# Performance work log

Measured on AMD Instinct MI355X. Metric: run time of the kernel, lower is better.

Reference implementation:

```python
import jax, jax.numpy as jnp
import numpy as np

NUM_LEVELS = 3      # init: nums_levels
SAMPLE_POINTS = 9   # init: sample_points (S+1 = 10 samples per level)


def _ste_ceil(x):
    # straight-through ceil: forward ceil(x), gradient identity
    return jnp.ceil(x) - jax.lax.stop_gradient(x) + x


def _ste_floor(x):
    return jnp.floor(x) - jax.lax.stop_gradient(x) + x


def _local_cost_volume(cv, cur_disp, radius, sample_nums):
    # cv: [B,D,H,W], cur_disp: [B,1,H,W]
    B, D, H, W = cv.shape
    lower = cur_disp - radius                                   # [B,1,H,W]
    interval = (2.0 * radius) / sample_nums                     # scalar (upper-lower)/S
    steps = jnp.arange(sample_nums + 1, dtype=cv.dtype).reshape(1, -1, 1, 1)
    cand = lower + steps * interval                             # [B,S+1,H,W]
    ceil_c = jnp.clip(_ste_ceil(cand), 0, D - 1)
    floor_c = jnp.clip(_ste_floor(cand), 0, D - 1)
    floor_rate = ceil_c - cand
    ceil_rate = 1.0 - floor_rate
    idx_c = jax.lax.stop_gradient(ceil_c).astype(jnp.int32)
    idx_f = jax.lax.stop_gradient(floor_c).astype(jnp.int32)
    vol_c = jnp.take_along_axis(cv, idx_c, axis=1)              # gather along D
    vol_f = jnp.take_along_axis(cv, idx_f, axis=1)
    return vol_c * ceil_rate + vol_f * floor_rate               # [B,S+1,H,W]


def setup_inputs() -> dict:
    key = jax.random.key(0)
    k1, k2 = jax.random.split(key)
    B, D, H, W = 16, 64, 128, 240
    cost_volume = jax.random.normal(k1, (B, D, H, W), dtype=jnp.float32)
    # current disparity estimate in [0, D-1)
    cur_disp = jax.random.uniform(k2, (B, 1, H, W), dtype=jnp.float32) * (D - 1)
    return {"cost_volume": cost_volume, "radius": 4, "cur_disp": cur_disp}


def reference(cost_volume, radius, cur_disp):
    # Build pyramid by pairwise averaging along the disparity dim
    # (equivalent to the permute + avg_pool1d(2,2) + permute in the original).
    pyramid = [cost_volume]
    cv = cost_volume
    for _ in range(NUM_LEVELS - 1):
        B, D, H, W = cv.shape
        cv = cv.reshape(B, D // 2, 2, H, W).mean(axis=2)
        pyramid.append(cv)
    outs = []
    for i in range(NUM_LEVELS):
        ref_disp = cur_disp / (2.0 ** i)
        outs.append(_local_cost_volume(pyramid[i], ref_disp, float(radius), SAMPLE_POINTS))
    return jnp.concatenate(outs, axis=1)  # [B, NUM_LEVELS*(S+1), H, W]
```

## Files before the change

### kernel.cpp

```cpp
#include <hip/hip_runtime.h>
#include <hip/hip_fp16.h>

#define BB 16
#define DD 64
#define HH 128
#define WW 240
#define HW (HH * WW)
#define NS 10
#define NL 3
#define BLK 256
#define NWORD (DD / 2)

__device__ inline unsigned pack2h(float lo, float hi) {
    __half2 h = __floats2half2_rn(lo, hi);
    return *reinterpret_cast<unsigned*>(&h);
}
__device__ inline float2 unpack2h(unsigned u) {
    __half2 h = *reinterpret_cast<__half2*>(&u);
    return __half22float2(h);
}
__device__ inline float exth(unsigned u, int sel) {
    unsigned short us = (unsigned short)(u >> (sel << 4));
    __half_raw hr; hr.x = us;
    return __half2float(*reinterpret_cast<__half*>(&hr));
}

__global__ __launch_bounds__(BLK, 4) void pcv_kernel(
    const float* __restrict__ cv,
    const int* __restrict__ radius_p,
    const float* __restrict__ disp_in,
    float* __restrict__ out)
{
    __shared__ unsigned ldsw[NWORD * BLK];
    const int tid = threadIdx.x;
    const int p = blockIdx.x * BLK + tid;
    const int b = p / HW;
    const int pix = p - b * HW;

    const float disp = disp_in[p];

    const float r = (float)(*radius_p);
    const float interval = (float)((2.0 * (double)r) / 9.0);

    {
        const int pixbase = blockIdx.x * BLK - b * HW;
        const float* src = cv + (size_t)b * DD * HW + pixbase;
        const int q = tid & 63;
        const int jbase = tid >> 6;
        #pragma unroll
        for (int it = 0; it < 8; ++it) {
            const int j = it * 4 + jbase;
            float4 v0 = *reinterpret_cast<const float4*>(src + (size_t)(2 * j)     * HW + q * 4);
            float4 v1 = *reinterpret_cast<const float4*>(src + (size_t)(2 * j + 1) * HW + q * 4);
            uint4 wv;
            wv.x = pack2h(v0.x, v1.x);
            wv.y = pack2h(v0.y, v1.y);
            wv.z = pack2h(v0.z, v1.z);
            wv.w = pack2h(v0.w, v1.w);
            *reinterpret_cast<uint4*>(&ldsw[j * BLK + q * 4]) = wv;
        }
    }
    __syncthreads();

    float* outp = out + (size_t)b * (NL * NS) * HW + pix;

    float rd = disp;
    int Dl = DD;
    #pragma unroll
    for (int lvl = 0; lvl < NL; ++lvl) {
        const float lower = rd - r;
        const float dmax = (float)(Dl - 1);
        #pragma unroll
        for (int s = 0; s < NS; ++s) {
            float cand = lower + (float)s * interval;
            float cc = fminf(fmaxf(ceilf(cand),  0.0f), dmax);
            float fc = fminf(fmaxf(floorf(cand), 0.0f), dmax);
            float fr = cc - cand;
            float cr = 1.0f - fr;
            int ic = (int)cc;
            int fi = (int)fc;
            float vc, vf;
            if (lvl == 0) {
                unsigned uf = ldsw[(fi >> 1) * BLK + tid];
                unsigned uc = ldsw[(ic >> 1) * BLK + tid];
                vf = exth(uf, fi & 1);
                vc = exth(uc, ic & 1);
            } else if (lvl == 1) {
                float2 a = unpack2h(ldsw[fi * BLK + tid]);
                float2 c = unpack2h(ldsw[ic * BLK + tid]);
                vf = 0.5f * (a.x + a.y);
                vc = 0.5f * (c.x + c.y);
            } else {
                float2 a0 = unpack2h(ldsw[(2 * fi)     * BLK + tid]);
                float2 a1 = unpack2h(ldsw[(2 * fi + 1) * BLK + tid]);
                float2 c0 = unpack2h(ldsw[(2 * ic)     * BLK + tid]);
                float2 c1 = unpack2h(ldsw[(2 * ic + 1) * BLK + tid]);
                vf = 0.5f * (0.5f * (a0.x + a0.y) + 0.5f * (a1.x + a1.y));
                vc = 0.5f * (0.5f * (c0.x + c0.y) + 0.5f * (c1.x + c1.y));
            }
            outp[(size_t)(lvl * NS + s) * HW] = vc * cr + vf * fr;
        }
        rd *= 0.5f;
        Dl >>= 1;
    }
}

extern "C" void kernel_launch(void* const* d_in, const int* in_sizes, int n_in,
                              void* d_out, int out_size, void* d_ws, size_t ws_size,
                              hipStream_t stream) {
    const float* cv     = (const float*)d_in[0];
    const int*   radius = (const int*)  d_in[1];
    const float* disp   = (const float*)d_in[2];
    float*       out    = (float*)d_out;

    const int npix = BB * HH * WW;
    pcv_kernel<<<dim3(npix / BLK), dim3(BLK), 0, stream>>>(cv, radius, disp, out);
}
```

Baseline: 34.65 us.

## Make kernel persistent with register prefetch and double-buffered LDS tiles

Launches a fixed grid of 512 blocks that loop over pixel tiles. While the current tile is computed from one LDS buffer, the next tile's cost-volume slice and disparity are loaded into registers, and they are packed into the other LDS buffer on the following iteration. This aims to overlap global loads with the gather/interpolate and store phase. In exchange it doubles LDS per block, holds 64 extra registers for prefetch, and has uneven tile counts per block.

Result: slower. 37.32 us (+7.7%).

```diff
diff --git a/kernel.cpp b/kernel.cpp
--- a/kernel.cpp
+++ b/kernel.cpp
@@ -10,6 +10,8 @@
 #define NL 3
 #define BLK 256
 #define NWORD (DD / 2)
+#define GRID 512
+#define NTILE (BB * HW / BLK)
 
 __device__ inline unsigned pack2h(float lo, float hi) {
     __half2 h = __floats2half2_rn(lo, hi);
@@ -25,83 +27,119 @@
     return __half2float(*reinterpret_cast<__half*>(&hr));
 }
 
-__global__ __launch_bounds__(BLK, 4) void pcv_kernel(
+__global__ __launch_bounds__(BLK) void pcv_kernel(
     const float* __restrict__ cv,
     const int* __restrict__ radius_p,
     const float* __restrict__ disp_in,
     float* __restrict__ out)
 {
-    __shared__ unsigned ldsw[NWORD * BLK];
+    __shared__ unsigned ldsw[2][NWORD * BLK];
     const int tid = threadIdx.x;
-    const int p = blockIdx.x * BLK + tid;
-    const int b = p / HW;
-    const int pix = p - b * HW;
-
-    const float disp = disp_in[p];
+    const int bid = blockIdx.x;
+    const int q  = tid & 63;
+    const int jb = tid >> 6;
 
     const float r = (float)(*radius_p);
     const float interval = (float)((2.0 * (double)r) / 9.0);
 
+    const int ntiles = (NTILE - bid + GRID - 1) / GRID;
+
+    float4 rv[16];
+    float  dsp;
+
     {
-        const int pixbase = blockIdx.x * BLK - b * HW;
+        const int t = bid;
+        const int pb = t * BLK;
+        const int b = pb / HW;
+        const int pixbase = pb - b * HW;
         const float* src = cv + (size_t)b * DD * HW + pixbase;
-        const int q = tid & 63;
-        const int jbase = tid >> 6;
         #pragma unroll
         for (int it = 0; it < 8; ++it) {
-            const int j = it * 4 + jbase;
-            float4 v0 = *reinterpret_cast<const float4*>(src + (size_t)(2 * j)     * HW + q * 4);
-            float4 v1 = *reinterpret_cast<const float4*>(src + (size_t)(2 * j + 1) * HW + q * 4);
+            const int j = it * 4 + jb;
+            rv[2 * it]     = *reinterpret_cast<const float4*>(src + (size_t)(2 * j)     * HW + q * 4);
+            rv[2 * it + 1] = *reinterpret_cast<const float4*>(src + (size_t)(2 * j + 1) * HW + q * 4);
+        }
+        dsp = disp_in[pb + tid];
+    }
+
+    int cur = 0;
+    for (int k = 0; k < ntiles; ++k) {
+        const int t = bid + k * GRID;
+        const int pb = t * BLK;
+        const int b = pb / HW;
+        const int pix = pb - b * HW + tid;
+
+        unsigned* buf = &ldsw[cur][0];
+        #pragma unroll
+        for (int it = 0; it < 8; ++it) {
+            const int j = it * 4 + jb;
             uint4 wv;
-            wv.x = pack2h(v0.x, v1.x);
-            wv.y = pack2h(v0.y, v1.y);
-            wv.z = pack2h(v0.z, v1.z);
-            wv.w = pack2h(v0.w, v1.w);
-            *reinterpret_cast<uint4*>(&ldsw[j * BLK + q * 4]) = wv;
+            wv.x = pack2h(rv[2 * it].x, rv[2 * it + 1].x);
+            wv.y = pack2h(rv[2 * it].y, rv[2 * it + 1].y);
+            wv.z = pack2h(rv[2 * it].z, rv[2 * it + 1].z);
+            wv.w = pack2h(rv[2 * it].w, rv[2 * it + 1].w);
+            *reinterpret_cast<uint4*>(&buf[j * BLK + q * 4]) = wv;
         }
-    }
-    __syncthreads();
+        const float disp = dsp;
 
-    float* outp = out + (size_t)b * (NL * NS) * HW + pix;
+        if (k + 1 < ntiles) {
+            const int tn = bid + (k + 1) * GRID;
+            const int pbn = tn * BLK;
+            const int bn = pbn / HW;
+            const int pixbase_n = pbn - bn * HW;
+            const float* srcn = cv + (size_t)bn * DD * HW + pixbase_n;
+            #pragma unroll
+            for (int it = 0; it < 8; ++it) {
+                const int j = it * 4 + jb;
+                rv[2 * it]     = *reinterpret_cast<const float4*>(srcn + (size_t)(2 * j)     * HW + q * 4);
+                rv[2 * it + 1] = *reinterpret_cast<const float4*>(srcn + (size_t)(2 * j + 1) * HW + q * 4);
+            }
+            dsp = disp_in[pbn + tid];
+        }
 
-    float rd = disp;
-    int Dl = DD;
-    #pragma unroll
-    for (int lvl = 0; lvl < NL; ++lvl) {
-        const float lower = rd - r;
-        const float dmax = (float)(Dl - 1);
+        asm volatile("s_waitcnt lgkmcnt(0)\n\ts_barrier" ::: "memory");
+
+        float* outp = out + (size_t)b * (NL * NS) * HW + pix;
+        float rd = disp;
+        int Dl = DD;
         #pragma unroll
-        for (int s = 0; s < NS; ++s) {
-            float cand = lower + (float)s * interval;
-            float cc = fminf(fmaxf(ceilf(cand),  0.0f), dmax);
-            float fc = fminf(fmaxf(floorf(cand), 0.0f), dmax);
-            float fr = cc - cand;
-            float cr = 1.0f - fr;
-            int ic = (int)cc;
-            int fi = (int)fc;
-            float vc, vf;
-            if (lvl == 0) {
-                unsigned uf = ldsw[(fi >> 1) * BLK + tid];
-                unsigned uc = ldsw[(ic >> 1) * BLK + tid];
-                vf = exth(uf, fi & 1);
-                vc = exth(uc, ic & 1);
-            } else if (lvl == 1) {
-                float2 a = unpack2h(ldsw[fi * BLK + tid]);
-                float2 c = unpack2h(ldsw[ic * BLK + tid]);
-                vf = 0.5f * (a.x + a.y);
-                vc = 0.5f * (c.x + c.y);
-            } else {
-                float2 a0 = unpack2h(ldsw[(2 * fi)     * BLK + tid]);
-                float2 a1 = unpack2h(ldsw[(2 * fi + 1) * BLK + tid]);
-                float2 c0 = unpack2h(ldsw[(2 * ic)     * BLK + tid]);
-                float2 c1 = unpack2h(ldsw[(2 * ic + 1) * BLK + tid]);
-                vf = 0.5f * (0.5f * (a0.x + a0.y) + 0.5f * (a1.x + a1.y));
-                vc = 0.5f * (0.5f * (c0.x + c0.y) + 0.5f * (c1.x + c1.y));
+        for (int lvl = 0; lvl < NL; ++lvl) {
+            const float lower = rd - r;
+            const float dmax = (float)(Dl - 1);
+            #pragma unroll
+            for (int s = 0; s < NS; ++s) {
+                float cand = lower + (float)s * interval;
+                float cc = fminf(fmaxf(ceilf(cand),  0.0f), dmax);
+                float fc = fminf(fmaxf(floorf(cand), 0.0f), dmax);
+                float fr = cc - cand;
+                float cr = 1.0f - fr;
+                int ic = (int)cc;
+                int fi = (int)fc;
+                float vc, vf;
+                if (lvl == 0) {
+                    unsigned uf = buf[(fi >> 1) * BLK + tid];
+                    unsigned uc = buf[(ic >> 1) * BLK + tid];
+                    vf = exth(uf, fi & 1);
+                    vc = exth(uc, ic & 1);
+                } else if (lvl == 1) {
+                    float2 a = unpack2h(buf[fi * BLK + tid]);
+                    float2 c = unpack2h(buf[ic * BLK + tid]);
+                    vf = 0.5f * (a.x + a.y);
+                    vc = 0.5f * (c.x + c.y);
+                } else {
+                    float2 a0 = unpack2h(buf[(2 * fi)     * BLK + tid]);
+                    float2 a1 = unpack2h(buf[(2 * fi + 1) * BLK + tid]);
+                    float2 c0 = unpack2h(buf[(2 * ic)     * BLK + tid]);
+                    float2 c1 = unpack2h(buf[(2 * ic + 1) * BLK + tid]);
+                    vf = 0.5f * (0.5f * (a0.x + a0.y) + 0.5f * (a1.x + a1.y));
+                    vc = 0.5f * (0.5f * (c0.x + c0.y) + 0.5f * (c1.x + c1.y));
+                }
+                outp[(size_t)(lvl * NS + s) * HW] = vc * cr + vf * fr;
             }
-            outp[(size_t)(lvl * NS + s) * HW] = vc * cr + vf * fr;
+            rd *= 0.5f;
+            Dl >>= 1;
         }
-        rd *= 0.5f;
-        Dl >>= 1;
+        cur ^= 1;
     }
 }
 
@@ -113,6 +151,5 @@
     const float* disp   = (const float*)d_in[2];
     float*       out    = (float*)d_out;
 
-    const int npix = BB * HH * WW;
-    pcv_kernel<<<dim3(npix / BLK), dim3(BLK), 0, stream>>>(cv, radius, disp, out);
+    pcv_kernel<<<dim3(GRID), dim3(BLK), 0, stream>>>(cv, radius, disp, out);
 }
```
